# Kernel optimization log

Measured on AMD Instinct MI355X. Metric: run time of the kernel, lower is better.

## Reference

```python
import jax, jax.numpy as jnp
import numpy as np
from jax import lax

B, S, T = 512, 64, 32
E, H = 512, 1024
VIN, VOUT = 128, 128


def gru_cell(x, h, W_ih, W_hh, b_ih, b_hh):
    # PyTorch GRU cell: gates ordered (r, z, n)
    gi = x @ W_ih.T + b_ih           # [B, 3*Hh]
    gh = h @ W_hh.T + b_hh           # [B, 3*Hh]
    i_r, i_z, i_n = jnp.split(gi, 3, axis=-1)
    h_r, h_z, h_n = jnp.split(gh, 3, axis=-1)
    r = jax.nn.sigmoid(i_r + h_r)
    z = jax.nn.sigmoid(i_z + h_z)
    n = jnp.tanh(i_n + r * h_n)
    return (1.0 - z) * n + z * h


def setup_inputs() -> dict:
    key = jax.random.key(0)
    ks = jax.random.split(key, 18)
    g = lambda k, shp: (jax.random.normal(k, shp, jnp.float32) * 0.05)
    return {
        "src": jax.random.randint(ks[0], (B, S), 0, VIN),
        "tgt": jax.random.randint(ks[1], (B, T), 0, VOUT),
        "enc_emb": g(ks[2], (VIN, E)),
        "dec_emb": g(ks[3], (VOUT, E)),
        "W_ih_f": g(ks[4], (3 * H, E)), "W_hh_f": g(ks[5], (3 * H, H)),
        "b_ih_f": g(ks[6], (3 * H,)), "b_hh_f": g(ks[7], (3 * H,)),
        "W_ih_b": g(ks[8], (3 * H, E)), "W_hh_b": g(ks[9], (3 * H, H)),
        "b_ih_b": g(ks[10], (3 * H,)), "b_hh_b": g(ks[11], (3 * H,)),
        "W_ih_d": g(ks[12], (3 * 2 * H, E)), "W_hh_d": g(ks[13], (3 * 2 * H, 2 * H)),
        "b_ih_d": g(ks[14], (3 * 2 * H,)), "b_hh_d": g(ks[15], (3 * 2 * H,)),
        "W_fc": g(ks[16], (VOUT, 2 * H)), "b_fc": g(ks[17], (VOUT,)),
    }


def reference(src, tgt, enc_emb, dec_emb,
              W_ih_f, W_hh_f, b_ih_f, b_hh_f,
              W_ih_b, W_hh_b, b_ih_b, b_hh_b,
              W_ih_d, W_hh_d, b_ih_d, b_hh_d,
              W_fc, b_fc):
    batch = src.shape[0]
    x = enc_emb[src]                         # [B, S, E]
    x_t = jnp.swapaxes(x, 0, 1)              # [S, B, E]

    def enc_scan(xs, W_ih, W_hh, b_ih, b_hh):
        h0 = jnp.zeros((batch, H), dtype=xs.dtype)
        def step(h, xt):
            h2 = gru_cell(xt, h, W_ih, W_hh, b_ih, b_hh)
            return h2, None
        hT, _ = lax.scan(step, h0, xs)
        return hT                             # final hidden [B, H]

    h_fwd = enc_scan(x_t, W_ih_f, W_hh_f, b_ih_f, b_hh_f)
    h_bwd = enc_scan(x_t[::-1], W_ih_b, W_hh_b, b_ih_b, b_hh_b)
    h = jnp.concatenate([h_fwd, h_bwd], axis=-1)   # [B, 2H] = torch.cat((h[-2], h[-1]), 1)

    tok0 = tgt[:, 0]                          # <sos> tokens

    def dec_step(carry, _):
        hh, tok = carry
        xt = dec_emb[tok]                     # [B, E]
        hh = gru_cell(xt, hh, W_ih_d, W_hh_d, b_ih_d, b_hh_d)
        logits = hh @ W_fc.T + b_fc           # [B, VOUT]
        nxt = jnp.argmax(logits, axis=-1)     # greedy feedback (teacher_forcing_ratio=0)
        return (hh, nxt), logits

    (_, _), logits = lax.scan(dec_step, (h, tok0), None, length=tgt.shape[1] - 1)
    return jnp.swapaxes(logits, 0, 1)         # [B, T-1, VOUT]
```

## Files before the change

### kernel.cpp

```cpp
#include <hip/hip_runtime.h>
#include <math.h>

#define B 512
#define S 64
#define T 32
#define E 512
#define H 1024
#define VOUTD 128
#define H2 (2*H)
#define H3 (3*H)
#define H6 (6*H)

typedef unsigned short ushortT;
typedef unsigned int uintT;
typedef __attribute__((ext_vector_type(8))) short short8;
typedef __attribute__((ext_vector_type(4))) float floatx4;

__device__ __forceinline__ float sigmoidf_(float x) { return 1.0f / (1.0f + expf(-x)); }

__device__ __forceinline__ uintT pack_hi2(float a, float b) {
    return (__float_as_uint(a) >> 16) | (__float_as_uint(b) & 0xFFFF0000u);
}
__device__ __forceinline__ uintT pack_lo2(float a, float b) {
    uintT ua = __float_as_uint(a), ub = __float_as_uint(b);
    uintT la = __float_as_uint(a - __uint_as_float(ua & 0xFFFF0000u)) >> 16;
    uintT lb = __float_as_uint(b - __uint_as_float(ub & 0xFFFF0000u)) >> 16;
    return la | (lb << 16);
}

__global__ __launch_bounds__(256) void zero16(uint4* __restrict__ p, int n)
{
    int i = blockIdx.x * 256 + threadIdx.x;
    if (i < n) p[i] = make_uint4(0u, 0u, 0u, 0u);
}

__global__ __launch_bounds__(256) void swizzle_w(
    const float* __restrict__ W, ushortT* __restrict__ out, int njShift, int kShift)
{
    const int K = 8 << kShift;
    const int nj = 1 << njShift;
    const int ncK = K >> 5;
    const int total = (nj >> 4) * ncK * 3;
    int f = blockIdx.x * 4 + (threadIdx.x >> 6);
    if (f >= total) return;
    const int lane = threadIdx.x & 63;
    int g = f % 3;
    int rest = f / 3;
    int c = rest & (ncK - 1);
    int jb = rest >> (kShift - 2);
    int jl = lane & 15, kq = lane >> 4;
    int row = g * nj + jb * 16 + jl;
    int k = c * 32 + kq * 8;
    const float* s = W + (size_t)row * K + k;
    float4 f0 = *(const float4*)s;
    float4 f1 = *(const float4*)(s + 4);
    uint4 hv = make_uint4(pack_hi2(f0.x, f0.y), pack_hi2(f0.z, f0.w),
                          pack_hi2(f1.x, f1.y), pack_hi2(f1.z, f1.w));
    uint4 lv = make_uint4(pack_lo2(f0.x, f0.y), pack_lo2(f0.z, f0.w),
                          pack_lo2(f1.x, f1.y), pack_lo2(f1.z, f1.w));
    size_t base = (size_t)f * 1024 + (size_t)lane * 8;
    *(uint4*)(out + base) = hv;
    *(uint4*)(out + base + 512) = lv;
}

#define MFMA16(a, b, c) __builtin_amdgcn_mfma_f32_16x16x32_bf16(a, b, c, 0, 0, 0)

#define LOADSET(SET, C)                                                         \
    {                                                                           \
        const ushortT* bp_ = bPtr + (size_t)(C) * 3072;                         \
        SET##b[0] = *(const short8*)(bp_);                                      \
        SET##b[1] = *(const short8*)(bp_ + 512);                                \
        SET##b[2] = *(const short8*)(bp_ + 1024);                               \
        SET##b[3] = *(const short8*)(bp_ + 1536);                               \
        SET##b[4] = *(const short8*)(bp_ + 2048);                               \
        SET##b[5] = *(const short8*)(bp_ + 2560);                               \
        _Pragma("unroll")                                                       \
        for (int rb_ = 0; rb_ < 4; ++rb_) {                                     \
            const ushortT* ap_ = aPtr + (size_t)rb_ * (NCKd * 1024)             \
                                      + (size_t)(C) * 1024;                     \
            SET##a[rb_ * 2]     = *(const short8*)(ap_);                        \
            SET##a[rb_ * 2 + 1] = *(const short8*)(ap_ + 512);                  \
        }                                                                       \
    }

#define COMPSET(SET)                                                            \
    _Pragma("unroll")                                                           \
    for (int g = 0; g < 3; ++g) {                                               \
        short8 bh_ = SET##b[g * 2], bl_ = SET##b[g * 2 + 1];                    \
        _Pragma("unroll")                                                       \
        for (int mi = 0; mi < 4; ++mi) {                                        \
            acc[mi][g] = MFMA16(SET##a[mi * 2], bh_, acc[mi][g]);               \
            acc[mi][g] = MFMA16(SET##a[mi * 2], bl_, acc[mi][g]);               \
            acc[mi][g] = MFMA16(SET##a[mi * 2 + 1], bh_, acc[mi][g]);           \
        }                                                                       \
    }

#define MAIN_LOOP()                                                             \
    LOADSET(s0, 0);                                                             \
    for (int c = 0; c < NCKd; c += 2) {                                         \
        LOADSET(s1, c + 1);                                                     \
        COMPSET(s0);                                                            \
        if (c + 2 < NCKd) LOADSET(s0, c + 2);                                   \
        COMPSET(s1);                                                            \
    }

#define EPILOGUE_STORE(NCKA)                                                    \
    __syncthreads();                                                            \
    {                                                                           \
        const int run = t >> 3;                                      \
        const int rb_ = run >> 1;                                    \
        const int pl_ = run & 1;                                     \
        const int sub = t & 7;                                                  \
        const ushortT* sp = &eb[rb_][pl_ * 256 + sub * 32];                     \
        ushortT* dp = AfrOut + (((size_t)((m0 >> 4) + rb_)) * (NCKA) + cA) * 1024 \
                    + pl_ * 512 + kqpar * 256 + sub * 32;                       \
        _Pragma("unroll")                                                       \
        for (int v = 0; v < 4; ++v)                                             \
            *(uint4*)(dp + v * 8) = *(const uint4*)(sp + v * 8);                \
    }

__global__ __launch_bounds__(256, 1) void fused_step_enc(
    const ushortT* __restrict__ Afr,
    const ushortT* __restrict__ WfrF, const ushortT* __restrict__ WfrB,
    const float* __restrict__ giTabF, const float* __restrict__ giTabB,
    const int* __restrict__ src, int s,
    const float* __restrict__ bhF, const float* __restrict__ bhB,
    float* __restrict__ h, ushortT* __restrict__ AfrOut)
{
    __shared__ ushortT eb[16][512];
    const int t = threadIdx.x, lane = t & 63, w = t >> 6;
    const int bid = blockIdx.x;
    const int xcd = bid & 7, q = bid >> 3;
    const int jg16 = xcd * 8 + (q & 7);
    const int mb   = q >> 3;
    const int j0 = jg16 * 16, m0 = mb * 256;
    const bool bwd = (m0 >= B);
    const ushortT* Wfr = bwd ? WfrB : WfrF;
    const float* giTab = bwd ? giTabB : giTabF;
    const float* bh = bwd ? bhB : bhF;
    const int NCKd = 32;
    const int sidx = bwd ? (S - 1 - s) : s;

    const ushortT* aPtr = Afr + (size_t)((m0 >> 4) + w * 4) * (NCKd * 1024) + lane * 8;
    const ushortT* bPtr = Wfr + (size_t)jg16 * (NCKd * 3072) + lane * 8;

    floatx4 acc[4][3];
#pragma unroll
    for (int mi = 0; mi < 4; ++mi)
#pragma unroll
        for (int g = 0; g < 3; ++g) acc[mi][g] = (floatx4){0.f, 0.f, 0.f, 0.f};

    short8 s0b[6], s0a[8], s1b[6], s1a[8];
    MAIN_LOOP();

    const int colj = j0 + (lane & 15);
    const float bR = bh[colj], bZ = bh[H + colj], bN = bh[2 * H + colj];
    const int cA = jg16 >> 1;
    const int kqpar = jg16 & 1;
    const int khalf = (lane >> 3) & 1;
    const int e7 = lane & 7;
#pragma unroll
    for (int mi = 0; mi < 4; ++mi) {
#pragma unroll
        for (int r = 0; r < 4; ++r) {
            const int r15 = (lane >> 4) * 4 + r;
            const int row = m0 + w * 64 + mi * 16 + r15;
            const int tk = src[(row & (B - 1)) * S + sidx];
            const float* gi = giTab + (size_t)tk * H3;
            float ghr = acc[mi][0][r] + bR;
            float ghz = acc[mi][1][r] + bZ;
            float ghn = acc[mi][2][r] + bN;
            float rr = sigmoidf_(gi[colj] + ghr);
            float z  = sigmoidf_(gi[H + colj] + ghz);
            float n  = tanhf(gi[2 * H + colj] + rr * ghn);
            const size_t idx = (size_t)row * H + colj;
            float hnew = (1.0f - z) * n + z * h[idx];
            h[idx] = hnew;
            uintT u = __float_as_uint(hnew);
            const int slot = (r15 + 16 * khalf) * 8 + e7;
            eb[w * 4 + mi][slot] = (ushortT)(u >> 16);
            eb[w * 4 + mi][256 + slot] =
                (ushortT)(__float_as_uint(hnew - __uint_as_float(u & 0xFFFF0000u)) >> 16);
        }
    }
    EPILOGUE_STORE(32)
}

__global__ __launch_bounds__(256, 1) void fused_step_dec(
    const ushortT* __restrict__ Afr, const ushortT* __restrict__ Wfr,
    const float* __restrict__ giTabD, const int* __restrict__ tok,
    const float* __restrict__ bhD,
    float* __restrict__ h, ushortT* __restrict__ AfrOut)
{
    __shared__ ushortT eb[16][512];
    const int t = threadIdx.x, lane = t & 63, w = t >> 6;
    const int bid = blockIdx.x;
    const int xcd = bid & 7, q = bid >> 3;
    const int jg16 = xcd * 16 + (q & 15);
    const int mb   = q >> 4;
    const int j0 = jg16 * 16, m0 = mb * 256;
    const int NCKd = 64;

    const ushortT* aPtr = Afr + (size_t)((m0 >> 4) + w * 4) * (NCKd * 1024) + lane * 8;
    const ushortT* bPtr = Wfr + (size_t)jg16 * (NCKd * 3072) + lane * 8;

    floatx4 acc[4][3];
#pragma unroll
    for (int mi = 0; mi < 4; ++mi)
#pragma unroll
        for (int g = 0; g < 3; ++g) acc[mi][g] = (floatx4){0.f, 0.f, 0.f, 0.f};

    short8 s0b[6], s0a[8], s1b[6], s1a[8];
    MAIN_LOOP();

    const int colj = j0 + (lane & 15);
    const float bR = bhD[colj], bZ = bhD[H2 + colj], bN = bhD[2 * H2 + colj];
    const int cA = jg16 >> 1;
    const int kqpar = jg16 & 1;
    const int khalf = (lane >> 3) & 1;
    const int e7 = lane & 7;
#pragma unroll
    for (int mi = 0; mi < 4; ++mi) {
#pragma unroll
        for (int r = 0; r < 4; ++r) {
            const int r15 = (lane >> 4) * 4 + r;
            const int row = m0 + w * 64 + mi * 16 + r15;
            const float* gi = giTabD + (size_t)tok[row] * H6;
            float ghr = acc[mi][0][r] + bR;
            float ghz = acc[mi][1][r] + bZ;
            float ghn = acc[mi][2][r] + bN;
            float rr = sigmoidf_(gi[colj] + ghr);
            float z  = sigmoidf_(gi[H2 + colj] + ghz);
            float n  = tanhf(gi[2 * H2 + colj] + rr * ghn);
            const size_t idx = (size_t)row * H2 + colj;
            float hnew = (1.0f - z) * n + z * h[idx];
            h[idx] = hnew;
            uintT u = __float_as_uint(hnew);
            const int slot = (r15 + 16 * khalf) * 8 + e7;
            eb[w * 4 + mi][slot] = (ushortT)(u >> 16);
            eb[w * 4 + mi][256 + slot] =
                (ushortT)(__float_as_uint(hnew - __uint_as_float(u & 0xFFFF0000u)) >> 16);
        }
    }
    EPILOGUE_STORE(64)
}

__global__ __launch_bounds__(256) void init_hh_tok_split(
    const float* __restrict__ h_f, const float* __restrict__ h_b,
    const int* __restrict__ tgt, float* __restrict__ hh,
    ushortT* __restrict__ AfrD, int* __restrict__ tok)
{
    int i = blockIdx.x * blockDim.x + threadIdx.x;
    int b = i >> 11;
    int j = i & 2047;
    float v = (j < H) ? h_f[(size_t)b * H + j] : h_b[(size_t)b * H + (j - H)];
    hh[i] = v;
    uintT u = __float_as_uint(v);
    size_t ao = (((size_t)(b >> 4) * 64 + (j >> 5)) * 2) * 512
              + (size_t)((b & 15) + 16 * ((j >> 3) & 3)) * 8 + (j & 7);
    AfrD[ao] = (ushortT)(u >> 16);
    AfrD[ao + 512] = (ushortT)(__float_as_uint(v - __uint_as_float(u & 0xFFFF0000u)) >> 16);
    if (j == 0) tok[b] = tgt[b * T];
}

__global__ __launch_bounds__(256) void logits_argmax2(
    const float* __restrict__ hh, const float* __restrict__ W_fc,
    const float* __restrict__ b_fc, float* __restrict__ out,
    int* __restrict__ tok, int t)
{
    __shared__ float sh[2][H2];
    __shared__ float sred[2][2][128];
    __shared__ float sval[2][128];
    __shared__ int   sidx[2][128];
    const int tid = threadIdx.x;
    const int col = tid & 127;
    const int kh  = tid >> 7;
    const int b0  = blockIdx.x * 2;

    {
        const float4* srcp = (const float4*)(hh + (size_t)b0 * H2);
        float4* dst = (float4*)sh;
        for (int i = tid; i < 2 * H2 / 4; i += 256) dst[i] = srcp[i];
    }
    __syncthreads();

    const float* wrow = W_fc + (size_t)col * H2 + kh * (H2 / 2);
    const float* s0 = sh[0] + kh * (H2 / 2);
    const float* s1 = sh[1] + kh * (H2 / 2);
    float a0 = 0.f, a1 = 0.f;
#pragma unroll 8
    for (int k = 0; k < H2 / 2; k += 4) {
        float4 w4 = *(const float4*)(wrow + k);
        float4 h0 = *(const float4*)(s0 + k);
        float4 h1 = *(const float4*)(s1 + k);
        a0 += w4.x * h0.x + w4.y * h0.y + w4.z * h0.z + w4.w * h0.w;
        a1 += w4.x * h1.x + w4.y * h1.y + w4.z * h1.z + w4.w * h1.w;
    }
    sred[kh][0][col] = a0;
    sred[kh][1][col] = a1;
    __syncthreads();

    if (kh == 0) {
        float l0 = sred[0][0][col] + sred[1][0][col] + b_fc[col];
        float l1 = sred[0][1][col] + sred[1][1][col] + b_fc[col];
        out[(size_t)(b0 + 0) * ((T - 1) * VOUTD) + (size_t)t * VOUTD + col] = l0;
        out[(size_t)(b0 + 1) * ((T - 1) * VOUTD) + (size_t)t * VOUTD + col] = l1;
        sval[0][col] = l0; sidx[0][col] = col;
        sval[1][col] = l1; sidx[1][col] = col;
    }
    __syncthreads();

    const int r = tid >> 7, c = tid & 127;
    for (int off = 64; off > 0; off >>= 1) {
        if (c < off) {
            float ov = sval[r][c + off]; int oi = sidx[r][c + off];
            if (ov > sval[r][c] || (ov == sval[r][c] && oi < sidx[r][c])) {
                sval[r][c] = ov; sidx[r][c] = oi;
            }
        }
        __syncthreads();
    }
    if (tid < 2) tok[b0 + tid] = sidx[tid][0];
}

__global__ __launch_bounds__(256) void gemm_sk(
    const float* __restrict__ Abase, int lda,
    const float* __restrict__ W, float* __restrict__ Cp, int N, int K, int KS)
{
    __shared__ float As[16][68];
    __shared__ float Ws[16][68];
    const int t = threadIdx.x;
    const int m0 = blockIdx.y * 64, n0 = blockIdx.x * 64;
    const int Kc = K / KS, kb = blockIdx.z * Kc;
    const int lr = t >> 2, lc = (t & 3) << 2;
    const int tx = t & 15, ty = t >> 4;
    const int tn0 = tx << 2, tm0 = ty << 2;
    const float* Aptr = Abase + (size_t)(m0 + lr) * lda + kb;
    const float* Wptr = W + (size_t)(n0 + lr) * K + kb;
    float acc[4][4] = {{0.f}};
    for (int k0 = 0; k0 < Kc; k0 += 16) {
        float4 a4 = *(const float4*)(Aptr + k0 + lc);
        float4 w4 = *(const float4*)(Wptr + k0 + lc);
        __syncthreads();
        As[lc+0][lr] = a4.x; As[lc+1][lr] = a4.y; As[lc+2][lr] = a4.z; As[lc+3][lr] = a4.w;
        Ws[lc+0][lr] = w4.x; Ws[lc+1][lr] = w4.y; Ws[lc+2][lr] = w4.z; Ws[lc+3][lr] = w4.w;
        __syncthreads();
#pragma unroll
        for (int kk = 0; kk < 16; ++kk) {
            float4 av = *(const float4*)&As[kk][tm0];
            float4 wv = *(const float4*)&Ws[kk][tn0];
            float am[4] = {av.x, av.y, av.z, av.w};
            float wn[4] = {wv.x, wv.y, wv.z, wv.w};
#pragma unroll
            for (int i = 0; i < 4; ++i)
#pragma unroll
                for (int j = 0; j < 4; ++j) acc[i][j] += am[i] * wn[j];
        }
    }
    float* Cb = Cp + ((size_t)blockIdx.z * VOUTD + m0 + tm0) * N + n0 + tn0;
#pragma unroll
    for (int i = 0; i < 4; ++i)
        *(float4*)(Cb + (size_t)i * N) = make_float4(acc[i][0], acc[i][1], acc[i][2], acc[i][3]);
}

__global__ __launch_bounds__(256) void gi_combine(
    const float* __restrict__ Cp, const float* __restrict__ bias,
    float* __restrict__ Cout, int N, int KS)
{
    int j = blockIdx.x * 256 + threadIdx.x;
    int v = blockIdx.y;
    float s = 0.f;
    for (int z = 0; z < KS; ++z) s += Cp[((size_t)z * VOUTD + v) * N + j];
    Cout[(size_t)v * N + j] = s + bias[j];
}

__global__ __launch_bounds__(256) void gemm_bias(
    const float* __restrict__ Abase,
    const int* __restrict__ idx, int idxStride, int idxOff, int lda,
    const float* __restrict__ W, const float* __restrict__ bias,
    float* __restrict__ C, int N, int K)
{
    __shared__ float As[16][68];
    __shared__ float Ws[16][68];
    const int t = threadIdx.x;
    const int m0 = blockIdx.y * 64, n0 = blockIdx.x * 64;
    const int lr = t >> 2, lc = (t & 3) << 2;
    const int tx = t & 15, ty = t >> 4;
    const int tn0 = tx << 2, tm0 = ty << 2;
    const int arow = m0 + lr;
    const float* Aptr = idx ? (Abase + (size_t)idx[arow * idxStride + idxOff] * lda)
                            : (Abase + (size_t)arow * lda);
    const float* Wptr = W + (size_t)(n0 + lr) * K;
    float acc[4][4] = {{0.f}};
    for (int k0 = 0; k0 < K; k0 += 16) {
        float4 a4 = *(const float4*)(Aptr + k0 + lc);
        float4 w4 = *(const float4*)(Wptr + k0 + lc);
        __syncthreads();
        As[lc+0][lr] = a4.x; As[lc+1][lr] = a4.y; As[lc+2][lr] = a4.z; As[lc+3][lr] = a4.w;
        Ws[lc+0][lr] = w4.x; Ws[lc+1][lr] = w4.y; Ws[lc+2][lr] = w4.z; Ws[lc+3][lr] = w4.w;
        __syncthreads();
#pragma unroll
        for (int kk = 0; kk < 16; ++kk) {
            float4 av = *(const float4*)&As[kk][tm0];
            float4 wv = *(const float4*)&Ws[kk][tn0];
            float am[4] = {av.x, av.y, av.z, av.w};
            float wn[4] = {wv.x, wv.y, wv.z, wv.w};
#pragma unroll
            for (int i = 0; i < 4; ++i)
#pragma unroll
                for (int j = 0; j < 4; ++j) acc[i][j] += am[i] * wn[j];
        }
    }
    const float b0 = bias[n0+tn0], b1 = bias[n0+tn0+1], b2 = bias[n0+tn0+2], b3 = bias[n0+tn0+3];
#pragma unroll
    for (int i = 0; i < 4; ++i) {
        float4 o = make_float4(acc[i][0]+b0, acc[i][1]+b1, acc[i][2]+b2, acc[i][3]+b3);
        *(float4*)(C + (size_t)(m0 + tm0 + i) * N + n0 + tn0) = o;
    }
}

__global__ __launch_bounds__(256) void gemm_enc(
    const float* __restrict__ Abase, int lda, int K,
    const int* __restrict__ srcIdx, int s,
    const float* __restrict__ W1, const float* __restrict__ bias1,
    const float* __restrict__ W2, const float* __restrict__ bias2,
    float* __restrict__ C, int N)
{
    __shared__ float As[16][68];
    __shared__ float Ws[16][68];
    const int t = threadIdx.x;
    const int m0 = blockIdx.y * 64, n0 = blockIdx.x * 64;
    const bool bwd = (m0 >= B);
    const float* W = bwd ? W2 : W1;
    const float* bias = bwd ? bias2 : bias1;
    const int lr = t >> 2, lc = (t & 3) << 2;
    const int tx = t & 15, ty = t >> 4;
    const int tn0 = tx << 2, tm0 = ty << 2;
    const int arow = m0 + lr;
    const float* Aptr;
    if (srcIdx) {
        int r = arow & (B - 1);
        int sidx = bwd ? (S - 1 - s) : s;
        Aptr = Abase + (size_t)srcIdx[r * S + sidx] * lda;
    } else Aptr = Abase + (size_t)arow * lda;
    const float* Wptr = W + (size_t)(n0 + lr) * K;
    float acc[4][4] = {{0.f}};
    for (int k0 = 0; k0 < K; k0 += 16) {
        float4 a4 = *(const float4*)(Aptr + k0 + lc);
        float4 w4 = *(const float4*)(Wptr + k0 + lc);
        __syncthreads();
        As[lc+0][lr] = a4.x; As[lc+1][lr] = a4.y; As[lc+2][lr] = a4.z; As[lc+3][lr] = a4.w;
        Ws[lc+0][lr] = w4.x; Ws[lc+1][lr] = w4.y; Ws[lc+2][lr] = w4.z; Ws[lc+3][lr] = w4.w;
        __syncthreads();
#pragma unroll
        for (int kk = 0; kk < 16; ++kk) {
            float4 av = *(const float4*)&As[kk][tm0];
            float4 wv = *(const float4*)&Ws[kk][tn0];
            float am[4] = {av.x, av.y, av.z, av.w};
            float wn[4] = {wv.x, wv.y, wv.z, wv.w};
#pragma unroll
            for (int i = 0; i < 4; ++i)
#pragma unroll
                for (int j = 0; j < 4; ++j) acc[i][j] += am[i] * wn[j];
        }
    }
    const float b0 = bias[n0+tn0], b1 = bias[n0+tn0+1], b2 = bias[n0+tn0+2], b3 = bias[n0+tn0+3];
#pragma unroll
    for (int i = 0; i < 4; ++i) {
        float4 o = make_float4(acc[i][0]+b0, acc[i][1]+b1, acc[i][2]+b2, acc[i][3]+b3);
        *(float4*)(C + (size_t)(m0 + tm0 + i) * N + n0 + tn0) = o;
    }
}

__global__ __launch_bounds__(256) void gru_gate(
    const float* __restrict__ gi, const float* __restrict__ gh,
    float* __restrict__ h, int Hd)
{
    int i = blockIdx.x * blockDim.x + threadIdx.x;
    int b = i / Hd, j = i - b * Hd;
    const float* gib = gi + (size_t)b * 3 * Hd;
    const float* ghb = gh + (size_t)b * 3 * Hd;
    float r = sigmoidf_(gib[j] + ghb[j]);
    float z = sigmoidf_(gib[Hd + j] + ghb[Hd + j]);
    float n = tanhf(gib[2 * Hd + j] + r * ghb[2 * Hd + j]);
    h[i] = (1.0f - z) * n + z * h[i];
}

__global__ __launch_bounds__(256) void init_hh_tok(
    const float* __restrict__ h_f, const float* __restrict__ h_b,
    const int* __restrict__ tgt, float* __restrict__ hh, int* __restrict__ tok)
{
    int i = blockIdx.x * blockDim.x + threadIdx.x;
    int b = i >> 11, j = i & 2047;
    hh[i] = (j < H) ? h_f[(size_t)b * H + j] : h_b[(size_t)b * H + (j - H)];
    if (j == 0) tok[b] = tgt[b * T];
}

extern "C" void kernel_launch(void* const* d_in, const int* in_sizes, int n_in,
                              void* d_out, int out_size, void* d_ws, size_t ws_size,
                              hipStream_t stream)
{
    const int*   src     = (const int*)d_in[0];
    const int*   tgt     = (const int*)d_in[1];
    const float* enc_emb = (const float*)d_in[2];
    const float* dec_emb = (const float*)d_in[3];
    const float* W_ih_f  = (const float*)d_in[4];
    const float* W_hh_f  = (const float*)d_in[5];
    const float* b_ih_f  = (const float*)d_in[6];
    const float* b_hh_f  = (const float*)d_in[7];
    const float* W_ih_b  = (const float*)d_in[8];
    const float* W_hh_b  = (const float*)d_in[9];
    const float* b_ih_b  = (const float*)d_in[10];
    const float* b_hh_b  = (const float*)d_in[11];
    const float* W_ih_d  = (const float*)d_in[12];
    const float* W_hh_d  = (const float*)d_in[13];
    const float* b_ih_d  = (const float*)d_in[14];
    const float* b_hh_d  = (const float*)d_in[15];
    const float* W_fc    = (const float*)d_in[16];
    const float* b_fc    = (const float*)d_in[17];
    float* out = (float*)d_out;

    char* base = (char*)d_ws;
    size_t off = 0;
    auto alloc = [&](size_t bytes) { char* p = base + off; off += (bytes + 255) & ~(size_t)255; return p; };

    float*   hE     = (float*)  alloc((size_t)2 * B * H * 4);
    ushortT* AfrEA  = (ushortT*)alloc((size_t)2 * B * H * 2 * 2);
    ushortT* AfrEB  = (ushortT*)alloc((size_t)2 * B * H * 2 * 2);
    float*   hh     = (float*)  alloc((size_t)B * H2 * 4);
    ushortT* AfrDA  = (ushortT*)alloc((size_t)B * H2 * 2 * 2);
    ushortT* AfrDB  = (ushortT*)alloc((size_t)B * H2 * 2 * 2);
    float*   giTabF = (float*)  alloc((size_t)VOUTD * H3 * 4);
    float*   giTabB = (float*)  alloc((size_t)VOUTD * H3 * 4);
    float*   giTabD = (float*)  alloc((size_t)VOUTD * H6 * 4);
    float*   giPart = (float*)  alloc((size_t)4 * VOUTD * H6 * 4);
    ushortT* WfrF   = (ushortT*)alloc((size_t)H3 * H * 2 * 2);
    ushortT* WfrB   = (ushortT*)alloc((size_t)H3 * H * 2 * 2);
    ushortT* WfrD   = (ushortT*)alloc((size_t)H6 * H2 * 2 * 2);
    int*     tok    = (int*)    alloc((size_t)B * 4);
    size_t required = off;

    dim3 blk(256);

    if (ws_size >= required) {
        {
            size_t zbytes = (size_t)2 * B * H * 4 + (size_t)2 * B * H * 4;
            int n16 = (int)(zbytes / 16);
            zero16<<<dim3((n16 + 255) / 256), blk, 0, stream>>>((uint4*)hE, n16);
        }
        {
            int fe = (H / 16) * (H / 32) * 3;
            int fd = (H2 / 16) * (H2 / 32) * 3;
            swizzle_w<<<dim3((fe + 3) / 4), blk, 0, stream>>>(W_hh_f, WfrF, 10, 7);
            swizzle_w<<<dim3((fe + 3) / 4), blk, 0, stream>>>(W_hh_b, WfrB, 10, 7);
            swizzle_w<<<dim3((fd + 3) / 4), blk, 0, stream>>>(W_hh_d, WfrD, 11, 8);
        }

        gemm_sk<<<dim3(H3 / 64, VOUTD / 64, 4), blk, 0, stream>>>(
            enc_emb, E, W_ih_f, giPart, H3, E, 4);
        gi_combine<<<dim3(H3 / 256, VOUTD), blk, 0, stream>>>(giPart, b_ih_f, giTabF, H3, 4);
        gemm_sk<<<dim3(H3 / 64, VOUTD / 64, 4), blk, 0, stream>>>(
            enc_emb, E, W_ih_b, giPart, H3, E, 4);
        gi_combine<<<dim3(H3 / 256, VOUTD), blk, 0, stream>>>(giPart, b_ih_b, giTabB, H3, 4);
        gemm_sk<<<dim3(H6 / 64, VOUTD / 64, 4), blk, 0, stream>>>(
            dec_emb, E, W_ih_d, giPart, H6, E, 4);
        gi_combine<<<dim3(H6 / 256, VOUTD), blk, 0, stream>>>(giPart, b_ih_d, giTabD, H6, 4);

        for (int s = 0; s < S; ++s) {
            const ushortT* inA = (s & 1) ? AfrEB : AfrEA;
            ushortT* outA = (s & 1) ? AfrEA : AfrEB;
            fused_step_enc<<<dim3(256), blk, 0, stream>>>(
                inA, WfrF, WfrB, giTabF, giTabB, src, s, b_hh_f, b_hh_b, hE, outA);
        }

        init_hh_tok_split<<<dim3((B * H2) / 256), blk, 0, stream>>>(
            hE, hE + (size_t)B * H, tgt, hh, AfrDA, tok);

        for (int t = 0; t < T - 1; ++t) {
            const ushortT* inA = (t & 1) ? AfrDB : AfrDA;
            ushortT* outA = (t & 1) ? AfrDA : AfrDB;
            fused_step_dec<<<dim3(256), blk, 0, stream>>>(
                inA, WfrD, giTabD, tok, b_hh_d, hh, outA);
            logits_argmax2<<<dim3(B / 2), blk, 0, stream>>>(hh, W_fc, b_fc, out, tok, t);
        }
    } else {
        {
            size_t zbytes = (size_t)2 * B * H * 4;
            int n16 = (int)(zbytes / 16);
            zero16<<<dim3((n16 + 255) / 256), blk, 0, stream>>>((uint4*)hE, n16);
        }
        float* giE = (float*)WfrF;
        float* ghF = giE + (size_t)2 * B * H3;
        dim3 grid_gi(H3 / 64, (2 * B) / 64);
        dim3 grid_gate((2 * B * H) / 256);
        for (int s = 0; s < S; ++s) {
            gemm_enc<<<grid_gi, blk, 0, stream>>>(enc_emb, E, E, src, s,
                                                  W_ih_f, b_ih_f, W_ih_b, b_ih_b, giE, H3);
            gemm_enc<<<grid_gi, blk, 0, stream>>>(hE, H, H, nullptr, 0,
                                                  W_hh_f, b_hh_f, W_hh_b, b_hh_b, ghF, H3);
            gru_gate<<<grid_gate, blk, 0, stream>>>(giE, ghF, hE, H);
        }
        init_hh_tok<<<dim3((B * H2) / 256), blk, 0, stream>>>(hE, hE + (size_t)B * H, tgt, hh, tok);
        dim3 grid_d(H6 / 64, B / 64);
        dim3 grid_dgate((B * H2) / 256);
        for (int t = 0; t < T - 1; ++t) {
            gemm_bias<<<grid_d, blk, 0, stream>>>(dec_emb, tok, 1, 0, E,
                                                  W_ih_d, b_ih_d, giE, H6, E);
            gemm_bias<<<grid_d, blk, 0, stream>>>(hh, nullptr, 0, 0, H2,
                                                  W_hh_d, b_hh_d, ghF, H6, H2);
            gru_gate<<<grid_dgate, blk, 0, stream>>>(giE, ghF, hh, H2);
            logits_argmax2<<<dim3(B / 2), blk, 0, stream>>>(hh, W_fc, b_fc, out, tok, t);
        }
    }
}
```

Before: 4.805 ms.

## Split K across two wave groups in fused GRU step kernels with LDS reduction

The fused encoder and decoder step kernels now launch 512 threads per block. Two groups of four waves each compute half of the K reduction, and the partial accumulators are summed through a shared-memory buffer before the gate epilogue. The goal is more waves per CU to hide memory latency in the recurrent GEMM, which has only 256 blocks per step. The cost is an extra 48KB of LDS per block, an added barrier and LDS round trip, and register pressure under launch_bounds(512,2).

```diff
diff --git a/kernel.cpp b/kernel.cpp
--- a/kernel.cpp
+++ b/kernel.cpp
@@ -97,29 +97,43 @@
 
 #define MAIN_LOOP()                                                             \
     LOADSET(s0, 0);                                                             \
-    for (int c = 0; c < NCKd; c += 2) {                                         \
+    for (int c = 0; c < NCKh; c += 2) {                                         \
         LOADSET(s1, c + 1);                                                     \
         COMPSET(s0);                                                            \
-        if (c + 2 < NCKd) LOADSET(s0, c + 2);                                   \
+        if (c + 2 < NCKh) LOADSET(s0, c + 2);                                   \
         COMPSET(s1);                                                            \
     }
 
-#define EPILOGUE_STORE(NCKA)                                                    \
+#define SPLITK_COMBINE()                                                        \
+    if (kh == 1) {                                                              \
+        _Pragma("unroll")                                                       \
+        for (int mi = 0; mi < 4; ++mi)                                          \
+            _Pragma("unroll")                                                   \
+            for (int g = 0; g < 3; ++g) part[wr][mi * 3 + g][lane] = acc[mi][g];\
+    }                                                                           \
+    __syncthreads();                                                            \
+    if (kh == 0) {                                                              \
+        _Pragma("unroll")                                                       \
+        for (int mi = 0; mi < 4; ++mi)                                          \
+            _Pragma("unroll")                                                   \
+            for (int g = 0; g < 3; ++g) acc[mi][g] = acc[mi][g] + part[wr][mi * 3 + g][lane]; \
+    }
+
+#define EPILOGUE_STORE512(NCKA)                                                 \
     __syncthreads();                                                            \
     {                                                                           \
-        const int run = t >> 3;                                      \
+        const int run = t >> 4;                                      \
         const int rb_ = run >> 1;                                    \
         const int pl_ = run & 1;                                     \
-        const int sub = t & 7;                                                  \
-        const ushortT* sp = &eb[rb_][pl_ * 256 + sub * 32];                     \
+        const int sub = t & 15;                                                 \
+        const ushortT* sp = &eb[rb_][pl_ * 256 + sub * 16];                     \
         ushortT* dp = AfrOut + (((size_t)((m0 >> 4) + rb_)) * (NCKA) + cA) * 1024 \
-                    + pl_ * 512 + kqpar * 256 + sub * 32;                       \
-        _Pragma("unroll")                                                       \
-        for (int v = 0; v < 4; ++v)                                             \
-            *(uint4*)(dp + v * 8) = *(const uint4*)(sp + v * 8);                \
-    }
-
-__global__ __launch_bounds__(256, 1) void fused_step_enc(
+                    + pl_ * 512 + kqpar * 256 + sub * 16;                       \
+        *(uint4*)(dp)     = *(const uint4*)(sp);                                \
+        *(uint4*)(dp + 8) = *(const uint4*)(sp + 8);                            \
+    }
+
+__global__ __launch_bounds__(512, 2) void fused_step_enc(
     const ushortT* __restrict__ Afr,
     const ushortT* __restrict__ WfrF, const ushortT* __restrict__ WfrB,
     const float* __restrict__ giTabF, const float* __restrict__ giTabB,
@@ -127,8 +141,10 @@
     const float* __restrict__ bhF, const float* __restrict__ bhB,
     float* __restrict__ h, ushortT* __restrict__ AfrOut)
 {
+    __shared__ floatx4 part[4][12][64];
     __shared__ ushortT eb[16][512];
     const int t = threadIdx.x, lane = t & 63, w = t >> 6;
+    const int wr = w & 3, kh = w >> 2;
     const int bid = blockIdx.x;
     const int xcd = bid & 7, q = bid >> 3;
     const int jg16 = xcd * 8 + (q & 7);
@@ -138,11 +154,13 @@
     const ushortT* Wfr = bwd ? WfrB : WfrF;
     const float* giTab = bwd ? giTabB : giTabF;
     const float* bh = bwd ? bhB : bhF;
-    const int NCKd = 32;
+    const int NCKd = 32, NCKh = 16;
     const int sidx = bwd ? (S - 1 - s) : s;
 
-    const ushortT* aPtr = Afr + (size_t)((m0 >> 4) + w * 4) * (NCKd * 1024) + lane * 8;
-    const ushortT* bPtr = Wfr + (size_t)jg16 * (NCKd * 3072) + lane * 8;
+    const ushortT* aPtr = Afr + (size_t)((m0 >> 4) + wr * 4) * (NCKd * 1024)
+                        + (size_t)kh * NCKh * 1024 + lane * 8;
+    const ushortT* bPtr = Wfr + (size_t)jg16 * (NCKd * 3072)
+                        + (size_t)kh * NCKh * 3072 + lane * 8;
 
     floatx4 acc[4][3];
 #pragma unroll
@@ -152,57 +170,64 @@
 
     short8 s0b[6], s0a[8], s1b[6], s1a[8];
     MAIN_LOOP();
-
-    const int colj = j0 + (lane & 15);
-    const float bR = bh[colj], bZ = bh[H + colj], bN = bh[2 * H + colj];
+    SPLITK_COMBINE();
+
     const int cA = jg16 >> 1;
     const int kqpar = jg16 & 1;
-    const int khalf = (lane >> 3) & 1;
-    const int e7 = lane & 7;
-#pragma unroll
-    for (int mi = 0; mi < 4; ++mi) {
-#pragma unroll
-        for (int r = 0; r < 4; ++r) {
-            const int r15 = (lane >> 4) * 4 + r;
-            const int row = m0 + w * 64 + mi * 16 + r15;
-            const int tk = src[(row & (B - 1)) * S + sidx];
-            const float* gi = giTab + (size_t)tk * H3;
-            float ghr = acc[mi][0][r] + bR;
-            float ghz = acc[mi][1][r] + bZ;
-            float ghn = acc[mi][2][r] + bN;
-            float rr = sigmoidf_(gi[colj] + ghr);
-            float z  = sigmoidf_(gi[H + colj] + ghz);
-            float n  = tanhf(gi[2 * H + colj] + rr * ghn);
-            const size_t idx = (size_t)row * H + colj;
-            float hnew = (1.0f - z) * n + z * h[idx];
-            h[idx] = hnew;
-            uintT u = __float_as_uint(hnew);
-            const int slot = (r15 + 16 * khalf) * 8 + e7;
-            eb[w * 4 + mi][slot] = (ushortT)(u >> 16);
-            eb[w * 4 + mi][256 + slot] =
-                (ushortT)(__float_as_uint(hnew - __uint_as_float(u & 0xFFFF0000u)) >> 16);
-        }
-    }
-    EPILOGUE_STORE(32)
-}
-
-__global__ __launch_bounds__(256, 1) void fused_step_dec(
+    if (kh == 0) {
+        const int colj = j0 + (lane & 15);
+        const float bR = bh[colj], bZ = bh[H + colj], bN = bh[2 * H + colj];
+        const int khalf = (lane >> 3) & 1;
+        const int e7 = lane & 7;
+#pragma unroll
+        for (int mi = 0; mi < 4; ++mi) {
+#pragma unroll
+            for (int r = 0; r < 4; ++r) {
+                const int r15 = (lane >> 4) * 4 + r;
+                const int row = m0 + wr * 64 + mi * 16 + r15;
+                const int tk = src[(row & (B - 1)) * S + sidx];
+                const float* gi = giTab + (size_t)tk * H3;
+                float ghr = acc[mi][0][r] + bR;
+                float ghz = acc[mi][1][r] + bZ;
+                float ghn = acc[mi][2][r] + bN;
+                float rr = sigmoidf_(gi[colj] + ghr);
+                float z  = sigmoidf_(gi[H + colj] + ghz);
+                float n  = tanhf(gi[2 * H + colj] + rr * ghn);
+                const size_t idx = (size_t)row * H + colj;
+                float hnew = (1.0f - z) * n + z * h[idx];
+                h[idx] = hnew;
+                uintT u = __float_as_uint(hnew);
+                const int slot = (r15 + 16 * khalf) * 8 + e7;
+                eb[wr * 4 + mi][slot] = (ushortT)(u >> 16);
+                eb[wr * 4 + mi][256 + slot] =
+                    (ushortT)(__float_as_uint(hnew - __uint_as_float(u & 0xFFFF0000u)) >> 16);
+            }
+        }
+    }
+    EPILOGUE_STORE512(32)
+}
+
+__global__ __launch_bounds__(512, 2) void fused_step_dec(
     const ushortT* __restrict__ Afr, const ushortT* __restrict__ Wfr,
     const float* __restrict__ giTabD, const int* __restrict__ tok,
     const float* __restrict__ bhD,
     float* __restrict__ h, ushortT* __restrict__ AfrOut)
 {
+    __shared__ floatx4 part[4][12][64];
     __shared__ ushortT eb[16][512];
     const int t = threadIdx.x, lane = t & 63, w = t >> 6;
+    const int wr = w & 3, kh = w >> 2;
     const int bid = blockIdx.x;
     const int xcd = bid & 7, q = bid >> 3;
     const int jg16 = xcd * 16 + (q & 15);
     const int mb   = q >> 4;
     const int j0 = jg16 * 16, m0 = mb * 256;
-    const int NCKd = 64;
-
-    const ushortT* aPtr = Afr + (size_t)((m0 >> 4) + w * 4) * (NCKd * 1024) + lane * 8;
-    const ushortT* bPtr = Wfr + (size_t)jg16 * (NCKd * 3072) + lane * 8;
+    const int NCKd = 64, NCKh = 32;
+
+    const ushortT* aPtr = Afr + (size_t)((m0 >> 4) + wr * 4) * (NCKd * 1024)
+                        + (size_t)kh * NCKh * 1024 + lane * 8;
+    const ushortT* bPtr = Wfr + (size_t)jg16 * (NCKd * 3072)
+                        + (size_t)kh * NCKh * 3072 + lane * 8;
 
     floatx4 acc[4][3];
 #pragma unroll
@@ -212,37 +237,40 @@
 
     short8 s0b[6], s0a[8], s1b[6], s1a[8];
     MAIN_LOOP();
-
-    const int colj = j0 + (lane & 15);
-    const float bR = bhD[colj], bZ = bhD[H2 + colj], bN = bhD[2 * H2 + colj];
+    SPLITK_COMBINE();
+
     const int cA = jg16 >> 1;
     const int kqpar = jg16 & 1;
-    const int khalf = (lane >> 3) & 1;
-    const int e7 = lane & 7;
-#pragma unroll
-    for (int mi = 0; mi < 4; ++mi) {
-#pragma unroll
-        for (int r = 0; r < 4; ++r) {
-            const int r15 = (lane >> 4) * 4 + r;
-            const int row = m0 + w * 64 + mi * 16 + r15;
-            const float* gi = giTabD + (size_t)tok[row] * H6;
-            float ghr = acc[mi][0][r] + bR;
-            float ghz = acc[mi][1][r] + bZ;
-            float ghn = acc[mi][2][r] + bN;
-            float rr = sigmoidf_(gi[colj] + ghr);
-            float z  = sigmoidf_(gi[H2 + colj] + ghz);
-            float n  = tanhf(gi[2 * H2 + colj] + rr * ghn);
-            const size_t idx = (size_t)row * H2 + colj;
-            float hnew = (1.0f - z) * n + z * h[idx];
-            h[idx] = hnew;
-            uintT u = __float_as_uint(hnew);
-            const int slot = (r15 + 16 * khalf) * 8 + e7;
-            eb[w * 4 + mi][slot] = (ushortT)(u >> 16);
-            eb[w * 4 + mi][256 + slot] =
-                (ushortT)(__float_as_uint(hnew - __uint_as_float(u & 0xFFFF0000u)) >> 16);
-        }
-    }
-    EPILOGUE_STORE(64)
+    if (kh == 0) {
+        const int colj = j0 + (lane & 15);
+        const float bR = bhD[colj], bZ = bhD[H2 + colj], bN = bhD[2 * H2 + colj];
+        const int khalf = (lane >> 3) & 1;
+        const int e7 = lane & 7;
+#pragma unroll
+        for (int mi = 0; mi < 4; ++mi) {
+#pragma unroll
+            for (int r = 0; r < 4; ++r) {
+                const int r15 = (lane >> 4) * 4 + r;
+                const int row = m0 + wr * 64 + mi * 16 + r15;
+                const float* gi = giTabD + (size_t)tok[row] * H6;
+                float ghr = acc[mi][0][r] + bR;
+                float ghz = acc[mi][1][r] + bZ;
+                float ghn = acc[mi][2][r] + bN;
+                float rr = sigmoidf_(gi[colj] + ghr);
+                float z  = sigmoidf_(gi[H2 + colj] + ghz);
+                float n  = tanhf(gi[2 * H2 + colj] + rr * ghn);
+                const size_t idx = (size_t)row * H2 + colj;
+                float hnew = (1.0f - z) * n + z * h[idx];
+                h[idx] = hnew;
+                uintT u = __float_as_uint(hnew);
+                const int slot = (r15 + 16 * khalf) * 8 + e7;
+                eb[wr * 4 + mi][slot] = (ushortT)(u >> 16);
+                eb[wr * 4 + mi][256 + slot] =
+                    (ushortT)(__float_as_uint(hnew - __uint_as_float(u & 0xFFFF0000u)) >> 16);
+            }
+        }
+    }
+    EPILOGUE_STORE512(64)
 }
 
 __global__ __launch_bounds__(256) void init_hh_tok_split(
@@ -541,6 +569,7 @@
     size_t required = off;
 
     dim3 blk(256);
+    dim3 blk512(512);
 
     if (ws_size >= required) {
         {
@@ -569,7 +598,7 @@
         for (int s = 0; s < S; ++s) {
             const ushortT* inA = (s & 1) ? AfrEB : AfrEA;
             ushortT* outA = (s & 1) ? AfrEA : AfrEB;
-            fused_step_enc<<<dim3(256), blk, 0, stream>>>(
+            fused_step_enc<<<dim3(256), blk512, 0, stream>>>(
                 inA, WfrF, WfrB, giTabF, giTabB, src, s, b_hh_f, b_hh_b, hE, outA);
         }
 
@@ -579,7 +608,7 @@
         for (int t = 0; t < T - 1; ++t) {
             const ushortT* inA = (t & 1) ? AfrDB : AfrDA;
             ushortT* outA = (t & 1) ? AfrDA : AfrDB;
-            fused_step_dec<<<dim3(256), blk, 0, stream>>>(
+            fused_step_dec<<<dim3(256), blk512, 0, stream>>>(
                 inA, WfrD, giTabD, tok, b_hh_d, hh, outA);
             logits_argmax2<<<dim3(B / 2), blk, 0, stream>>>(hh, W_fc, b_fc, out, tok, t);
         }
```

Result: faster. 4.616 ms (-3.9%).
